# Kernel optimization log

Measured on AMD Instinct MI355X. Metric: run time of the kernel, lower is better.

Reference implementation:

```python
import jax, jax.numpy as jnp
import numpy as np

N, B, T, E = 16384, 8, 32, 262144
D, H = 256, 8
HD = D // H

def _ln(x, g, b, eps=1e-5):
    m = x.mean(-1, keepdims=True)
    va = x.var(-1, keepdims=True)
    return (x - m) * jax.lax.rsqrt(va + eps) * g + b

def setup_inputs():
    key = jax.random.key(0)
    ks = jax.random.split(key, 40)
    rn = lambda i, sh, s=0.02: jax.random.normal(ks[i], sh, jnp.float32) * s
    inp = {}
    inp['x'] = jax.random.normal(ks[0], (N, D), jnp.float32)
    inp['edge_index'] = jax.random.randint(ks[1], (2, E), 0, N)
    inp['edge_attr'] = jax.random.normal(ks[2], (E, D), jnp.float32)
    inp['v'] = jax.random.normal(ks[3], (B, T, D), jnp.float32)
    inp['batch'] = jnp.sort(jax.random.randint(ks[4], (N,), 0, B))
    ones = lambda sh: jnp.ones(sh, jnp.float32)
    zeros = lambda sh: jnp.zeros(sh, jnp.float32)
    # LayerNorms
    inp['n1_g'], inp['n1_b'] = ones((D,)), zeros((D,))
    inp['vn_g'], inp['vn_b'] = ones((D,)), zeros((D,))
    inp['n3_g'], inp['n3_b'] = ones((D,)), zeros((D,))
    inp['n4_g'], inp['n4_b'] = ones((D,)), zeros((D,))
    # GINEConv: eps (train_eps, init 0) + MLP [D, 2D, D] with layer_norm+gelu on hidden
    inp['gine_eps'] = jnp.float32(0.0)
    inp['g_w1'], inp['g_b1'] = rn(5, (2 * D, D)), zeros((2 * D,))
    inp['g_lng'], inp['g_lnb'] = ones((2 * D,)), zeros((2 * D,))
    inp['g_w2'], inp['g_b2'] = rn(6, (D, 2 * D)), zeros((D,))
    # GatedResidual gammas (init 1e-5)
    inp['gamma1'] = jnp.full((D,), 1e-5, jnp.float32)
    inp['gamma2'] = jnp.full((D,), 1e-5, jnp.float32)
    inp['gamma3'] = jnp.full((D,), 1e-5, jnp.float32)
    # MultiheadAttention (packed in_proj)
    inp['mha_in_w'], inp['mha_in_b'] = rn(7, (3 * D, D)), zeros((3 * D,))
    inp['mha_out_w'], inp['mha_out_b'] = rn(8, (D, D)), zeros((D,))
    # node->token cross attention projections
    inp['q_w'], inp['q_b'] = rn(9, (D, D)), zeros((D,))
    inp['kv_w'], inp['kv_b'] = rn(10, (2 * D, D)), zeros((2 * D,))
    inp['o_w'], inp['o_b'] = rn(11, (D, D)), zeros((D,))
    # FFN MLP [D, 4D, D] (eval-mode batch_norm == identity with default stats)
    inp['f_w1'], inp['f_b1'] = rn(12, (4 * D, D)), zeros((4 * D,))
    inp['f_w2'], inp['f_b2'] = rn(13, (D, 4 * D)), zeros((D,))
    return inp

def reference(x, edge_index, edge_attr, v, batch,
              n1_g, n1_b, vn_g, vn_b, n3_g, n3_b, n4_g, n4_b,
              gine_eps, g_w1, g_b1, g_lng, g_lnb, g_w2, g_b2,
              gamma1, gamma2, gamma3,
              mha_in_w, mha_in_b, mha_out_w, mha_out_b,
              q_w, q_b, kv_w, kv_b, o_w, o_b,
              f_w1, f_b1, f_w2, f_b2):
    scale = HD ** -0.5
    gelu = lambda t: jax.nn.gelu(t, approximate=False)
    # --- GINEConv on norm1(x) ---
    xn = _ln(x, n1_g, n1_b)
    src, dst = edge_index[0], edge_index[1]
    msg = jax.nn.relu(xn[src] + edge_attr)                      # [E, D]
    agg = jax.ops.segment_sum(msg, dst, num_segments=N)         # [N, D]
    hin = (1.0 + gine_eps) * xn + agg
    h = gelu(_ln(hin @ g_w1.T + g_b1, g_lng, g_lnb)) @ g_w2.T + g_b2
    x = x + gamma1 * h                                          # res1 (drop_path off in eval)
    # --- token self-attention with node summary context ---
    v_res = v
    vn = _ln(v, vn_g, vn_b)
    cnt = jnp.maximum(jax.ops.segment_sum(jnp.ones((N,), x.dtype), batch, num_segments=B), 1.0)
    node_summary = jax.ops.segment_sum(x, batch, num_segments=B) / cnt[:, None]  # [B, D]
    ctx = jnp.concatenate([vn, node_summary[:, None, :]], axis=1)                # [B, T+1, D]
    wq, wk, wv = jnp.split(mha_in_w, 3, axis=0)
    bq, bk, bv = jnp.split(mha_in_b, 3, axis=0)
    qh = (vn @ wq.T + bq).reshape(B, T, H, HD)
    kh = (ctx @ wk.T + bk).reshape(B, T + 1, H, HD)
    vh = (ctx @ wv.T + bv).reshape(B, T + 1, H, HD)
    a = jax.nn.softmax(jnp.einsum('bqhd,bkhd->bhqk', qh, kh) * scale, axis=-1)
    v_upd = jnp.einsum('bhqk,bkhd->bqhd', a, vh).reshape(B, T, D) @ mha_out_w.T + mha_out_b
    v = v_res + gamma2 * v_upd                                  # res2
    # --- node -> token cross attention (gather-expand KV by batch) ---
    xn3 = _ln(x, n3_g, n3_b)
    q = (xn3 @ q_w.T + q_b).reshape(N, H, HD)
    kv = (v @ kv_w.T + kv_b).reshape(B, T, 2, H, HD)
    k, val = kv[:, :, 0], kv[:, :, 1]                           # [B, T, H, HD]
    k_exp, val_exp = k[batch], val[batch]                       # [N, T, H, HD]
    scores = jnp.einsum('nhd,nthd->nht', q, k_exp) * scale
    attn = jax.nn.softmax(scores, axis=-1)                      # scatter_softmax w/ all-zero idx == softmax over t
    attn_out = jnp.einsum('nht,nthd->nhd', attn, val_exp).reshape(N, D)
    x = x + gamma3 * (attn_out @ o_w.T + o_b)                   # res3
    # --- FFN ---
    xn4 = _ln(x, n4_g, n4_b)
    x = x + (gelu(xn4 @ f_w1.T + f_b1) @ f_w2.T + f_b2)
    return (x, v)
```

## Files before the change

### kernel.cpp

```cpp
#include <hip/hip_runtime.h>
#include <math.h>

#define NN 16384
#define EE 262144
#define BB 8
#define TT 32
#define DD 256
#define HH 8
#define HDD 32

typedef __bf16 bf16;
typedef __bf16 bf16x8 __attribute__((ext_vector_type(8)));
typedef __bf16 bf16x4 __attribute__((ext_vector_type(4)));
typedef float f32x4 __attribute__((ext_vector_type(4)));

#define GM_F32 0
#define GM_BF16 1
#define GM_GELU 2
#define GM_RES 3
#define GM_RES2 4

__device__ __forceinline__ float gelu_f(float v) {
  return 0.5f * v * (1.f + erff(v * 0.70710678118654752440f));
}

struct Cast9 {
  const float* src[9];
  bf16* dst[9];
  int blk_start[10];
};

__global__ __launch_bounds__(256) void cast9(Cast9 c) {
  int blk = blockIdx.x;
  int s = 0;
  while (blk >= c.blk_start[s + 1]) ++s;
  int local = blk - c.blk_start[s];
  int i = local * 1024 + threadIdx.x * 4;
  const float4 f = *(const float4*)(c.src[s] + i);
  bf16x4 o;
  o[0] = (bf16)f.x; o[1] = (bf16)f.y; o[2] = (bf16)f.z; o[3] = (bf16)f.w;
  *(bf16x4*)(c.dst[s] + i) = o;
}

__global__ __launch_bounds__(256) void zero_bufs(int* __restrict__ deg,
                                                 float* __restrict__ summary,
                                                 float* __restrict__ cntf) {
  int b = blockIdx.x;
  if (b < 64) deg[b * 256 + threadIdx.x] = 0;
  else if (b < 72) summary[(b - 64) * 256 + threadIdx.x] = 0.f;
  else if (threadIdx.x < BB) cntf[threadIdx.x] = 0.f;
}

__global__ __launch_bounds__(256) void ln_rows(const float* __restrict__ in,
                                               const float* __restrict__ g,
                                               const float* __restrict__ b,
                                               bf16* __restrict__ out, int C, int do_gelu) {
  int row = blockIdx.x;
  int t = threadIdx.x;
  const float* x = in + (size_t)row * C;
  int nc = C >> 8;
  float lv[2];
  float s = 0.f, s2 = 0.f;
  for (int j = 0; j < nc; ++j) {
    float v = x[j * 256 + t];
    lv[j] = v;
    s += v;
    s2 += v * v;
  }
#pragma unroll
  for (int o = 32; o > 0; o >>= 1) {
    s += __shfl_down(s, o, 64);
    s2 += __shfl_down(s2, o, 64);
  }
  __shared__ float red[8];
  int wv = t >> 6;
  if ((t & 63) == 0) { red[wv] = s; red[4 + wv] = s2; }
  __syncthreads();
  s = red[0] + red[1] + red[2] + red[3];
  s2 = red[4] + red[5] + red[6] + red[7];
  float m = s / C;
  float rs = rsqrtf(s2 / C - m * m + 1e-5f);
  for (int j = 0; j < nc; ++j) {
    int c = j * 256 + t;
    float v = (lv[j] - m) * rs * g[c] + b[c];
    if (do_gelu) v = gelu_f(v);
    out[(size_t)row * C + c] = (bf16)v;
  }
}

__global__ __launch_bounds__(256) void deg_count(const int* __restrict__ ei, int* __restrict__ deg) {
  int e = blockIdx.x * 256 + threadIdx.x;
  if (e < EE) atomicAdd(&deg[ei[EE + e]], 1);
}

__global__ __launch_bounds__(1024) void scan16k(const int* __restrict__ deg,
                                                int* __restrict__ offs, int* __restrict__ woff) {
  __shared__ int part[1024];
  int t = threadIdx.x;
  int base = t * 16;
  int v[16];
  int s = 0;
#pragma unroll
  for (int j = 0; j < 16; ++j) { v[j] = deg[base + j]; s += v[j]; }
  part[t] = s;
  __syncthreads();
  for (int o = 1; o < 1024; o <<= 1) {
    int x = (t >= o) ? part[t - o] : 0;
    __syncthreads();
    part[t] += x;
    __syncthreads();
  }
  int excl = part[t] - s;
#pragma unroll
  for (int j = 0; j < 16; ++j) {
    offs[base + j] = excl;
    woff[base + j] = excl;
    excl += v[j];
  }
  if (t == 1023) offs[NN] = part[1023];
}

__global__ __launch_bounds__(256) void csr_fill(const int* __restrict__ ei, int* __restrict__ woff,
                                                int2* __restrict__ csr2) {
  int e = blockIdx.x * 256 + threadIdx.x;
  if (e < EE) {
    int d = ei[EE + e];
    int s = ei[e];
    int p = atomicAdd(&woff[d], 1);
    csr2[p] = make_int2(e, s);
  }
}

__global__ __launch_bounds__(256) void gine_agg(const float* __restrict__ eattr,
                                                const bf16* __restrict__ xn,
                                                const int* __restrict__ offs,
                                                const int2* __restrict__ csr2,
                                                const float* __restrict__ epsp,
                                                bf16* __restrict__ hin) {
  __shared__ f32x4 red[4][64];
  int n = blockIdx.x;
  int wave = threadIdx.x >> 6, lane = threadIdx.x & 63;
  int s0 = offs[n], s1 = offs[n + 1];
  f32x4 acc = {0.f, 0.f, 0.f, 0.f};
  int i = s0 + wave;
  int2 es = (i < s1) ? csr2[i] : make_int2(0, 0);
  for (; i < s1; i += 4) {
    int2 cur = es;
    int inext = i + 4;
    if (inext < s1) es = csr2[inext];
    float4 ea = *(const float4*)(eattr + (size_t)cur.x * DD + lane * 4);
    bf16x4 xv = *(const bf16x4*)(xn + (size_t)cur.y * DD + lane * 4);
    acc[0] += fmaxf((float)xv[0] + ea.x, 0.f);
    acc[1] += fmaxf((float)xv[1] + ea.y, 0.f);
    acc[2] += fmaxf((float)xv[2] + ea.z, 0.f);
    acc[3] += fmaxf((float)xv[3] + ea.w, 0.f);
  }
  red[wave][lane] = acc;
  __syncthreads();
  if (wave == 0) {
    f32x4 a = red[0][lane];
    f32x4 a1 = red[1][lane], a2 = red[2][lane], a3 = red[3][lane];
    bf16x4 xs = *(const bf16x4*)(xn + (size_t)n * DD + lane * 4);
    float e1 = 1.f + epsp[0];
    bf16x4 o;
#pragma unroll
    for (int j = 0; j < 4; ++j)
      o[j] = (bf16)(e1 * (float)xs[j] + a[j] + a1[j] + a2[j] + a3[j]);
    *(bf16x4*)(hin + (size_t)n * DD + lane * 4) = o;
  }
}

__global__ __launch_bounds__(256) void gemm_bt(const bf16* __restrict__ A,
                                               const bf16* __restrict__ W,
                                               const float* __restrict__ bias,
                                               int M, int K, int NC, int mode,
                                               const float* __restrict__ res,
                                               const float* __restrict__ gamma,
                                               float* __restrict__ outf,
                                               bf16* __restrict__ outb) {
  int wave = threadIdx.x >> 6;
  int lane = threadIdx.x & 63;
  int qd = lane >> 4;
  int l16 = lane & 15;
  int r0 = blockIdx.y * 128 + wave * 32;
  int c0 = blockIdx.x * 64;
  int ar0 = r0 + l16;       if (ar0 >= M) ar0 = M - 1;
  int ar1 = r0 + 16 + l16;  if (ar1 >= M) ar1 = M - 1;
  const bf16* Ap0 = A + (size_t)ar0 * K + qd * 8;
  const bf16* Ap1 = A + (size_t)ar1 * K + qd * 8;
  const bf16* Wp = W + (size_t)(c0 + l16) * K + qd * 8;
  size_t K16 = (size_t)16 * K;
  f32x4 acc00 = {0.f, 0.f, 0.f, 0.f};
  f32x4 acc01 = acc00, acc02 = acc00, acc03 = acc00;
  f32x4 acc10 = acc00, acc11 = acc00, acc12 = acc00, acc13 = acc00;
  for (int k = 0; k < K; k += 32) {
    bf16x8 a0 = *(const bf16x8*)(Ap0 + k);
    bf16x8 a1 = *(const bf16x8*)(Ap1 + k);
    bf16x8 b0 = *(const bf16x8*)(Wp + k);
    bf16x8 b1 = *(const bf16x8*)(Wp + K16 + k);
    bf16x8 b2 = *(const bf16x8*)(Wp + 2 * K16 + k);
    bf16x8 b3 = *(const bf16x8*)(Wp + 3 * K16 + k);
    acc00 = __builtin_amdgcn_mfma_f32_16x16x32_bf16(a0, b0, acc00, 0, 0, 0);
    acc01 = __builtin_amdgcn_mfma_f32_16x16x32_bf16(a0, b1, acc01, 0, 0, 0);
    acc02 = __builtin_amdgcn_mfma_f32_16x16x32_bf16(a0, b2, acc02, 0, 0, 0);
    acc03 = __builtin_amdgcn_mfma_f32_16x16x32_bf16(a0, b3, acc03, 0, 0, 0);
    acc10 = __builtin_amdgcn_mfma_f32_16x16x32_bf16(a1, b0, acc10, 0, 0, 0);
    acc11 = __builtin_amdgcn_mfma_f32_16x16x32_bf16(a1, b1, acc11, 0, 0, 0);
    acc12 = __builtin_amdgcn_mfma_f32_16x16x32_bf16(a1, b2, acc12, 0, 0, 0);
    acc13 = __builtin_amdgcn_mfma_f32_16x16x32_bf16(a1, b3, acc13, 0, 0, 0);
  }
  f32x4 accs[2][4] = {{acc00, acc01, acc02, acc03}, {acc10, acc11, acc12, acc13}};
#pragma unroll
  for (int s = 0; s < 2; ++s) {
#pragma unroll
    for (int c = 0; c < 4; ++c) {
      int col = c0 + c * 16 + l16;
      float bv = bias[col];
#pragma unroll
      for (int i = 0; i < 4; ++i) {
        int row = r0 + s * 16 + qd * 4 + i;
        if (row >= M) continue;
        size_t idx = (size_t)row * NC + col;
        float v = accs[s][c][i] + bv;
        if (mode == GM_F32) outf[idx] = v;
        else if (mode == GM_BF16) outb[idx] = (bf16)v;
        else if (mode == GM_GELU) outb[idx] = (bf16)gelu_f(v);
        else {
          float g = gamma ? gamma[col] : 1.f;
          float r = res[idx] + g * v;
          outf[idx] = r;
          if (mode == GM_RES2) outb[idx] = (bf16)r;
        }
      }
    }
  }
}

__global__ __launch_bounds__(256) void cnt_kernel(const int* __restrict__ batch, float* __restrict__ cntf) {
  __shared__ int hist[BB];
  if (threadIdx.x < BB) hist[threadIdx.x] = 0;
  __syncthreads();
  int n = blockIdx.x * 256 + threadIdx.x;
  if (n < NN) atomicAdd(&hist[batch[n]], 1);
  __syncthreads();
  if (threadIdx.x < BB) {
    int h = hist[threadIdx.x];
    if (h) atomicAdd(&cntf[threadIdx.x], (float)h);
  }
}

__global__ __launch_bounds__(256) void seg_sum(const float* __restrict__ x1,
                                               const int* __restrict__ batch,
                                               float* __restrict__ summary) {
  int r0 = blockIdx.x * 64;
  int t = threadIdx.x;
  float acc = 0.f;
  int curb = batch[r0];
  for (int i = 0; i < 64; ++i) {
    int r = r0 + i;
    int b = batch[r];
    if (b != curb) {
      atomicAdd(&summary[(size_t)curb * DD + t], acc);
      acc = 0.f;
      curb = b;
    }
    acc += x1[(size_t)r * DD + t];
  }
  atomicAdd(&summary[(size_t)curb * DD + t], acc);
}

__global__ __launch_bounds__(256) void build_ctx(const float* __restrict__ summary,
                                                 const float* __restrict__ cntf,
                                                 const bf16* __restrict__ vn,
                                                 bf16* __restrict__ ctx) {
  int r = blockIdx.x, t = threadIdx.x;
  int b = r / (TT + 1), k = r % (TT + 1);
  float val;
  if (k < TT) val = (float)vn[((size_t)(b * TT + k)) * DD + t];
  else val = summary[(size_t)b * DD + t] / fmaxf(cntf[b], 1.f);
  ctx[(size_t)r * DD + t] = (bf16)val;
}

__global__ __launch_bounds__(256) void mha_small(const float* __restrict__ qh,
                                                 const float* __restrict__ kvh,
                                                 bf16* __restrict__ vatt) {
  int b = blockIdx.x;
  int h = threadIdx.x >> 5, qi = threadIdx.x & 31;
  const float scale = 0.17677669529663687f;
  float sc[TT + 1];
  float mx = -1e30f;
  const float* qp = qh + ((size_t)(b * TT + qi)) * DD + h * HDD;
#pragma unroll
  for (int k = 0; k < TT + 1; ++k) {
    const float* kp = kvh + ((size_t)(b * (TT + 1) + k)) * 512 + h * HDD;
    float s = 0.f;
#pragma unroll
    for (int d = 0; d < HDD; ++d) s += qp[d] * kp[d];
    s *= scale;
    sc[k] = s;
    mx = fmaxf(mx, s);
  }
  float sum = 0.f;
#pragma unroll
  for (int k = 0; k < TT + 1; ++k) {
    sc[k] = __expf(sc[k] - mx);
    sum += sc[k];
  }
  float inv = 1.f / sum;
#pragma unroll
  for (int d = 0; d < HDD; ++d) {
    float o = 0.f;
#pragma unroll
    for (int k = 0; k < TT + 1; ++k)
      o += sc[k] * kvh[((size_t)(b * (TT + 1) + k)) * 512 + 256 + h * HDD + d];
    vatt[((size_t)(b * TT + qi)) * DD + h * HDD + d] = (bf16)(o * inv);
  }
}

__global__ __launch_bounds__(256) void cross_attn(const bf16* __restrict__ qx,
                                                  const float* __restrict__ kvx,
                                                  const int* __restrict__ batch,
                                                  bf16* __restrict__ attnout) {
  __shared__ float v_lds[TT * DD];
  int tid = threadIdx.x;
  int n0 = blockIdx.x * 16;
  int b0 = batch[n0];
  for (int i = tid; i < TT * DD; i += 256) {
    int t = i >> 8, c = i & 255;
    v_lds[i] = kvx[((size_t)(b0 * TT + t)) * 512 + 256 + c];
  }
  int h = tid >> 5, lt = tid & 31;
  float kreg[HDD];
  {
    const float* kp = kvx + ((size_t)(b0 * TT + lt)) * 512 + h * HDD;
#pragma unroll
    for (int d = 0; d < HDD; ++d) kreg[d] = kp[d];
  }
  __syncthreads();
  const float scale = 0.17677669529663687f;
  for (int ni = 0; ni < 16; ++ni) {
    int n = n0 + ni;
    int b = batch[n];
    const bf16* qp = qx + (size_t)n * DD + h * HDD;
    float s = 0.f;
    if (b == b0) {
#pragma unroll
      for (int d = 0; d < HDD; ++d) s += (float)qp[d] * kreg[d];
    } else {
      const float* kp = kvx + ((size_t)(b * TT + lt)) * 512 + h * HDD;
#pragma unroll
      for (int d = 0; d < HDD; ++d) s += (float)qp[d] * kp[d];
    }
    s *= scale;
    float mx = s;
#pragma unroll
    for (int o = 16; o > 0; o >>= 1) mx = fmaxf(mx, __shfl_xor(mx, o, 32));
    float e = __expf(s - mx);
    float sum = e;
#pragma unroll
    for (int o = 16; o > 0; o >>= 1) sum += __shfl_xor(sum, o, 32);
    float a = e / sum;
    float o_acc = 0.f;
    int base_lane = (h & 1) << 5;
    if (b == b0) {
#pragma unroll
      for (int t = 0; t < TT; ++t) {
        float at = __shfl(a, base_lane + t, 64);
        o_acc += at * v_lds[t * DD + h * HDD + lt];
      }
    } else {
#pragma unroll
      for (int t = 0; t < TT; ++t) {
        float at = __shfl(a, base_lane + t, 64);
        o_acc += at * kvx[((size_t)(b * TT + t)) * 512 + 256 + h * HDD + lt];
      }
    }
    attnout[(size_t)n * DD + h * HDD + lt] = (bf16)o_acc;
  }
}

extern "C" void kernel_launch(void* const* d_in, const int* in_sizes, int n_in,
                              void* d_out, int out_size, void* d_ws, size_t ws_size,
                              hipStream_t stream) {
  const float* x = (const float*)d_in[0];
  const int* ei = (const int*)d_in[1];
  const float* eattr = (const float*)d_in[2];
  const float* v = (const float*)d_in[3];
  const int* batch = (const int*)d_in[4];
  const float* n1_g = (const float*)d_in[5];
  const float* n1_b = (const float*)d_in[6];
  const float* vn_g = (const float*)d_in[7];
  const float* vn_b = (const float*)d_in[8];
  const float* n3_g = (const float*)d_in[9];
  const float* n3_b = (const float*)d_in[10];
  const float* n4_g = (const float*)d_in[11];
  const float* n4_b = (const float*)d_in[12];
  const float* gine_eps = (const float*)d_in[13];
  const float* g_w1 = (const float*)d_in[14];
  const float* g_b1 = (const float*)d_in[15];
  const float* g_lng = (const float*)d_in[16];
  const float* g_lnb = (const float*)d_in[17];
  const float* g_w2 = (const float*)d_in[18];
  const float* g_b2 = (const float*)d_in[19];
  const float* gamma1 = (const float*)d_in[20];
  const float* gamma2 = (const float*)d_in[21];
  const float* gamma3 = (const float*)d_in[22];
  const float* mha_in_w = (const float*)d_in[23];
  const float* mha_in_b = (const float*)d_in[24];
  const float* mha_out_w = (const float*)d_in[25];
  const float* mha_out_b = (const float*)d_in[26];
  const float* q_w = (const float*)d_in[27];
  const float* q_b = (const float*)d_in[28];
  const float* kv_w = (const float*)d_in[29];
  const float* kv_b = (const float*)d_in[30];
  const float* o_w = (const float*)d_in[31];
  const float* o_b = (const float*)d_in[32];
  const float* f_w1 = (const float*)d_in[33];
  const float* f_b1 = (const float*)d_in[34];
  const float* f_w2 = (const float*)d_in[35];
  const float* f_b2 = (const float*)d_in[36];

  float* out_x = (float*)d_out;
  float* out_v = (float*)d_out + (size_t)NN * DD;

  char* wsp = (char*)d_ws;
  size_t off = 0;
  auto alloc = [&](size_t bytes) -> void* {
    void* p = wsp + off;
    off += (bytes + 255) & ~(size_t)255;
    return p;
  };
  float* t1f = (float*)alloc(33554432);
  bf16* u_bf = (bf16*)t1f;
  bf16* xn_bf = (bf16*)alloc(8388608);
  bf16* qx_bf = xn_bf;
  bf16* t1g_bf = (bf16*)alloc(16777216);
  float* x2f = (float*)t1g_bf;
  float* x1f = (float*)alloc(16777216);
  bf16* hin_bf = (bf16*)alloc(8388608);
  bf16* xn3_bf = hin_bf;
  bf16* att_bf = (bf16*)alloc(8388608);
  bf16* xn4_bf = att_bf;
  int* deg = (int*)alloc(NN * 4);
  int* offs = (int*)alloc((NN + 1) * 4);
  int* woff = (int*)alloc(NN * 4);
  int2* csr2 = (int2*)alloc((size_t)EE * 8);
  float* summary = (float*)alloc(BB * DD * 4);
  float* cntf = (float*)alloc(BB * 4);
  bf16* vn_bf = (bf16*)alloc(BB * TT * DD * 2);
  bf16* ctx_bf = (bf16*)alloc(BB * (TT + 1) * DD * 2);
  float* qhf = (float*)alloc(BB * TT * DD * 4);
  float* kvhf = (float*)alloc(BB * (TT + 1) * 512 * 4);
  bf16* vatt_bf = (bf16*)alloc(BB * TT * DD * 2);
  bf16* vout_bf = (bf16*)alloc(BB * TT * DD * 2);
  float* kvxf = (float*)alloc(BB * TT * 512 * 4);
  bf16* wbuf = (bf16*)alloc((size_t)1310720 * 2);

  bf16* g_w1b = wbuf;
  bf16* g_w2b = g_w1b + 131072;
  bf16* mha_in_wb = g_w2b + 131072;
  bf16* mha_out_wb = mha_in_wb + 196608;
  bf16* q_wb = mha_out_wb + 65536;
  bf16* kv_wb = q_wb + 65536;
  bf16* o_wb = kv_wb + 131072;
  bf16* f_w1b = o_wb + 65536;
  bf16* f_w2b = f_w1b + 262144;

  Cast9 cj;
  cj.src[0] = g_w1; cj.dst[0] = g_w1b;
  cj.src[1] = g_w2; cj.dst[1] = g_w2b;
  cj.src[2] = mha_in_w; cj.dst[2] = mha_in_wb;
  cj.src[3] = mha_out_w; cj.dst[3] = mha_out_wb;
  cj.src[4] = q_w; cj.dst[4] = q_wb;
  cj.src[5] = kv_w; cj.dst[5] = kv_wb;
  cj.src[6] = o_w; cj.dst[6] = o_wb;
  cj.src[7] = f_w1; cj.dst[7] = f_w1b;
  cj.src[8] = f_w2; cj.dst[8] = f_w2b;
  int bs[10] = {0, 128, 256, 448, 512, 576, 704, 768, 1024, 1280};
  for (int i = 0; i < 10; ++i) cj.blk_start[i] = bs[i];
  cast9<<<1280, 256, 0, stream>>>(cj);
  zero_bufs<<<73, 256, 0, stream>>>(deg, summary, cntf);

  ln_rows<<<NN, 256, 0, stream>>>(x, n1_g, n1_b, xn_bf, DD, 0);

  deg_count<<<EE / 256, 256, 0, stream>>>(ei, deg);
  scan16k<<<1, 1024, 0, stream>>>(deg, offs, woff);
  csr_fill<<<EE / 256, 256, 0, stream>>>(ei, woff, csr2);

  gine_agg<<<NN, 256, 0, stream>>>(eattr, xn_bf, offs, csr2, gine_eps, hin_bf);

  gemm_bt<<<dim3(8, 128), 256, 0, stream>>>(hin_bf, g_w1b, g_b1, NN, 256, 512, GM_F32,
                                            nullptr, nullptr, t1f, nullptr);
  ln_rows<<<NN, 256, 0, stream>>>(t1f, g_lng, g_lnb, t1g_bf, 512, 1);
  gemm_bt<<<dim3(4, 128), 256, 0, stream>>>(t1g_bf, g_w2b, g_b2, NN, 512, 256, GM_RES,
                                            x, gamma1, x1f, nullptr);

  cnt_kernel<<<NN / 256, 256, 0, stream>>>(batch, cntf);
  seg_sum<<<NN / 64, 256, 0, stream>>>(x1f, batch, summary);

  ln_rows<<<BB * TT, 256, 0, stream>>>(v, vn_g, vn_b, vn_bf, DD, 0);
  build_ctx<<<BB * (TT + 1), 256, 0, stream>>>(summary, cntf, vn_bf, ctx_bf);
  gemm_bt<<<dim3(4, 2), 256, 0, stream>>>(vn_bf, mha_in_wb, mha_in_b, BB * TT, 256, 256,
                                          GM_F32, nullptr, nullptr, qhf, nullptr);
  gemm_bt<<<dim3(8, 3), 256, 0, stream>>>(ctx_bf, mha_in_wb + (size_t)256 * 256,
                                          mha_in_b + 256, BB * (TT + 1), 256, 512,
                                          GM_F32, nullptr, nullptr, kvhf, nullptr);
  mha_small<<<BB, 256, 0, stream>>>(qhf, kvhf, vatt_bf);
  gemm_bt<<<dim3(4, 2), 256, 0, stream>>>(vatt_bf, mha_out_wb, mha_out_b, BB * TT, 256, 256,
                                          GM_RES2, v, gamma2, out_v, vout_bf);

  gemm_bt<<<dim3(8, 2), 256, 0, stream>>>(vout_bf, kv_wb, kv_b, BB * TT, 256, 512,
                                          GM_F32, nullptr, nullptr, kvxf, nullptr);
  ln_rows<<<NN, 256, 0, stream>>>(x1f, n3_g, n3_b, xn3_bf, DD, 0);
  gemm_bt<<<dim3(4, 128), 256, 0, stream>>>(xn3_bf, q_wb, q_b, NN, 256, 256, GM_BF16,
                                            nullptr, nullptr, nullptr, qx_bf);
  cross_attn<<<NN / 16, 256, 0, stream>>>(qx_bf, kvxf, batch, att_bf);
  gemm_bt<<<dim3(4, 128), 256, 0, stream>>>(att_bf, o_wb, o_b, NN, 256, 256, GM_RES,
                                            x1f, gamma3, x2f, nullptr);

  ln_rows<<<NN, 256, 0, stream>>>(x2f, n4_g, n4_b, xn4_bf, DD, 0);
  gemm_bt<<<dim3(16, 128), 256, 0, stream>>>(xn4_bf, f_w1b, f_b1, NN, 256, 1024, GM_GELU,
                                             nullptr, nullptr, nullptr, u_bf);
  gemm_bt<<<dim3(4, 128), 256, 0, stream>>>(u_bf, f_w2b, f_b2, NN, 1024, 256, GM_RES,
                                            x2f, nullptr, out_x, nullptr);
}
```

Measured before the change: 959.7 us.

## Merge independent small kernels into combined launches and double-buffer GEMM loads

Several independent kernels (weight casts, two LayerNorms, batch histogram, degree count) are folded into one prologue launch dispatched by block index. Seg-sum is merged with the n3 LayerNorm, the ctx build with the q projection GEMM, and the gine W1 GEMM with the small MHA q GEMM, which cuts launch count and per-kernel tail idle time. The GEMM inner loop is also unrolled by two with explicit register double-buffering so global loads for the next K step are issued before the current MFMAs. Zeroing now uses a single memset. The costs are higher register pressure in the GEMM and heterogeneous blocks sharing one launch.

```diff
diff --git a/kernel.cpp b/kernel.cpp
--- a/kernel.cpp
+++ b/kernel.cpp
@@ -24,73 +24,70 @@
   return 0.5f * v * (1.f + erff(v * 0.70710678118654752440f));
 }
 
-struct Cast9 {
-  const float* src[9];
-  bf16* dst[9];
-  int blk_start[10];
-};
-
-__global__ __launch_bounds__(256) void cast9(Cast9 c) {
-  int blk = blockIdx.x;
-  int s = 0;
-  while (blk >= c.blk_start[s + 1]) ++s;
-  int local = blk - c.blk_start[s];
-  int i = local * 1024 + threadIdx.x * 4;
-  const float4 f = *(const float4*)(c.src[s] + i);
-  bf16x4 o;
-  o[0] = (bf16)f.x; o[1] = (bf16)f.y; o[2] = (bf16)f.z; o[3] = (bf16)f.w;
-  *(bf16x4*)(c.dst[s] + i) = o;
-}
-
-__global__ __launch_bounds__(256) void zero_bufs(int* __restrict__ deg,
-                                                 float* __restrict__ summary,
-                                                 float* __restrict__ cntf) {
-  int b = blockIdx.x;
-  if (b < 64) deg[b * 256 + threadIdx.x] = 0;
-  else if (b < 72) summary[(b - 64) * 256 + threadIdx.x] = 0.f;
-  else if (threadIdx.x < BB) cntf[threadIdx.x] = 0.f;
-}
-
-__global__ __launch_bounds__(256) void ln_rows(const float* __restrict__ in,
-                                               const float* __restrict__ g,
-                                               const float* __restrict__ b,
-                                               bf16* __restrict__ out, int C, int do_gelu) {
-  int row = blockIdx.x;
+__device__ __forceinline__ void ln256(const float* __restrict__ xr,
+                                      const float* __restrict__ g,
+                                      const float* __restrict__ bb,
+                                      bf16* __restrict__ o, float* red) {
   int t = threadIdx.x;
-  const float* x = in + (size_t)row * C;
-  int nc = C >> 8;
-  float lv[2];
-  float s = 0.f, s2 = 0.f;
-  for (int j = 0; j < nc; ++j) {
-    float v = x[j * 256 + t];
-    lv[j] = v;
-    s += v;
-    s2 += v * v;
-  }
-#pragma unroll
-  for (int o = 32; o > 0; o >>= 1) {
-    s += __shfl_down(s, o, 64);
-    s2 += __shfl_down(s2, o, 64);
-  }
-  __shared__ float red[8];
+  float v = xr[t];
+  float s = v, s2 = v * v;
+#pragma unroll
+  for (int off = 32; off > 0; off >>= 1) {
+    s += __shfl_down(s, off, 64);
+    s2 += __shfl_down(s2, off, 64);
+  }
   int wv = t >> 6;
   if ((t & 63) == 0) { red[wv] = s; red[4 + wv] = s2; }
   __syncthreads();
   s = red[0] + red[1] + red[2] + red[3];
   s2 = red[4] + red[5] + red[6] + red[7];
-  float m = s / C;
-  float rs = rsqrtf(s2 / C - m * m + 1e-5f);
-  for (int j = 0; j < nc; ++j) {
-    int c = j * 256 + t;
-    float v = (lv[j] - m) * rs * g[c] + b[c];
-    if (do_gelu) v = gelu_f(v);
-    out[(size_t)row * C + c] = (bf16)v;
-  }
-}
-
-__global__ __launch_bounds__(256) void deg_count(const int* __restrict__ ei, int* __restrict__ deg) {
-  int e = blockIdx.x * 256 + threadIdx.x;
-  if (e < EE) atomicAdd(&deg[ei[EE + e]], 1);
+  float m = s * (1.f / 256.f);
+  float rs = rsqrtf(s2 * (1.f / 256.f) - m * m + 1e-5f);
+  o[t] = (bf16)((v - m) * rs * g[t] + bb[t]);
+}
+
+struct Pro {
+  const float* wsrc[9];
+  bf16* wdst[9];
+  int wblk[10];
+  const float* x; const float* n1_g; const float* n1_b; bf16* xn;
+  const float* v; const float* vn_g; const float* vn_b; bf16* vn;
+  const int* batch; float* cntf;
+  const int* ei; int* deg;
+};
+
+__global__ __launch_bounds__(256) void prologue(Pro p) {
+  __shared__ float red[8];
+  __shared__ int hist[BB];
+  int b = blockIdx.x, t = threadIdx.x;
+  if (b < 1280) {
+    int s = 0;
+    while (b >= p.wblk[s + 1]) ++s;
+    int i = (b - p.wblk[s]) * 1024 + t * 4;
+    const float4 f = *(const float4*)(p.wsrc[s] + i);
+    bf16x4 o;
+    o[0] = (bf16)f.x; o[1] = (bf16)f.y; o[2] = (bf16)f.z; o[3] = (bf16)f.w;
+    *(bf16x4*)(p.wdst[s] + i) = o;
+  } else if (b < 17664) {
+    size_t r = b - 1280;
+    ln256(p.x + r * 256, p.n1_g, p.n1_b, p.xn + r * 256, red);
+  } else if (b < 17920) {
+    size_t r = b - 17664;
+    ln256(p.v + r * 256, p.vn_g, p.vn_b, p.vn + r * 256, red);
+  } else if (b < 17984) {
+    if (t < BB) hist[t] = 0;
+    __syncthreads();
+    int n = (b - 17920) * 256 + t;
+    atomicAdd(&hist[p.batch[n]], 1);
+    __syncthreads();
+    if (t < BB) {
+      int h = hist[t];
+      if (h) atomicAdd(&p.cntf[t], (float)h);
+    }
+  } else {
+    int e = (b - 17984) * 256 + t;
+    atomicAdd(&p.deg[p.ei[EE + e]], 1);
+  }
 }
 
 __global__ __launch_bounds__(1024) void scan16k(const int* __restrict__ deg,
@@ -170,115 +167,174 @@
   }
 }
 
-__global__ __launch_bounds__(256) void gemm_bt(const bf16* __restrict__ A,
-                                               const bf16* __restrict__ W,
-                                               const float* __restrict__ bias,
-                                               int M, int K, int NC, int mode,
-                                               const float* __restrict__ res,
-                                               const float* __restrict__ gamma,
-                                               float* __restrict__ outf,
-                                               bf16* __restrict__ outb) {
+struct GemmP {
+  const bf16* A; const bf16* W; const float* bias;
+  int M, K, NC, mode;
+  const float* res; const float* gamma;
+  float* outf; bf16* outb;
+};
+
+__device__ __forceinline__ void gemm_core(const GemmP p, int bx, int by) {
   int wave = threadIdx.x >> 6;
   int lane = threadIdx.x & 63;
   int qd = lane >> 4;
   int l16 = lane & 15;
-  int r0 = blockIdx.y * 128 + wave * 32;
-  int c0 = blockIdx.x * 64;
-  int ar0 = r0 + l16;       if (ar0 >= M) ar0 = M - 1;
-  int ar1 = r0 + 16 + l16;  if (ar1 >= M) ar1 = M - 1;
-  const bf16* Ap0 = A + (size_t)ar0 * K + qd * 8;
-  const bf16* Ap1 = A + (size_t)ar1 * K + qd * 8;
-  const bf16* Wp = W + (size_t)(c0 + l16) * K + qd * 8;
-  size_t K16 = (size_t)16 * K;
+  int r0 = by * 128 + wave * 32;
+  int c0 = bx * 64;
+  int ar0 = r0 + l16;       if (ar0 >= p.M) ar0 = p.M - 1;
+  int ar1 = r0 + 16 + l16;  if (ar1 >= p.M) ar1 = p.M - 1;
+  const bf16* Ap0 = p.A + (size_t)ar0 * p.K + qd * 8;
+  const bf16* Ap1 = p.A + (size_t)ar1 * p.K + qd * 8;
+  const bf16* Wp = p.W + (size_t)(c0 + l16) * p.K + qd * 8;
+  size_t K16 = (size_t)16 * p.K;
   f32x4 acc00 = {0.f, 0.f, 0.f, 0.f};
   f32x4 acc01 = acc00, acc02 = acc00, acc03 = acc00;
   f32x4 acc10 = acc00, acc11 = acc00, acc12 = acc00, acc13 = acc00;
-  for (int k = 0; k < K; k += 32) {
-    bf16x8 a0 = *(const bf16x8*)(Ap0 + k);
-    bf16x8 a1 = *(const bf16x8*)(Ap1 + k);
-    bf16x8 b0 = *(const bf16x8*)(Wp + k);
-    bf16x8 b1 = *(const bf16x8*)(Wp + K16 + k);
-    bf16x8 b2 = *(const bf16x8*)(Wp + 2 * K16 + k);
-    bf16x8 b3 = *(const bf16x8*)(Wp + 3 * K16 + k);
-    acc00 = __builtin_amdgcn_mfma_f32_16x16x32_bf16(a0, b0, acc00, 0, 0, 0);
-    acc01 = __builtin_amdgcn_mfma_f32_16x16x32_bf16(a0, b1, acc01, 0, 0, 0);
-    acc02 = __builtin_amdgcn_mfma_f32_16x16x32_bf16(a0, b2, acc02, 0, 0, 0);
-    acc03 = __builtin_amdgcn_mfma_f32_16x16x32_bf16(a0, b3, acc03, 0, 0, 0);
-    acc10 = __builtin_amdgcn_mfma_f32_16x16x32_bf16(a1, b0, acc10, 0, 0, 0);
-    acc11 = __builtin_amdgcn_mfma_f32_16x16x32_bf16(a1, b1, acc11, 0, 0, 0);
-    acc12 = __builtin_amdgcn_mfma_f32_16x16x32_bf16(a1, b2, acc12, 0, 0, 0);
-    acc13 = __builtin_amdgcn_mfma_f32_16x16x32_bf16(a1, b3, acc13, 0, 0, 0);
-  }
+  bf16x8 a0, a1, b0, b1, b2, b3, na0, na1, nb0, nb1, nb2, nb3;
+
+#define GLOADS(A0, A1, B0, B1, B2, B3, kk)                \
+  A0 = *(const bf16x8*)(Ap0 + (kk));                      \
+  A1 = *(const bf16x8*)(Ap1 + (kk));                      \
+  B0 = *(const bf16x8*)(Wp + (kk));                       \
+  B1 = *(const bf16x8*)(Wp + K16 + (kk));                 \
+  B2 = *(const bf16x8*)(Wp + 2 * K16 + (kk));             \
+  B3 = *(const bf16x8*)(Wp + 3 * K16 + (kk));
+#define GMFMAS(A0, A1, B0, B1, B2, B3)                                  \
+  acc00 = __builtin_amdgcn_mfma_f32_16x16x32_bf16(A0, B0, acc00, 0, 0, 0); \
+  acc01 = __builtin_amdgcn_mfma_f32_16x16x32_bf16(A0, B1, acc01, 0, 0, 0); \
+  acc02 = __builtin_amdgcn_mfma_f32_16x16x32_bf16(A0, B2, acc02, 0, 0, 0); \
+  acc03 = __builtin_amdgcn_mfma_f32_16x16x32_bf16(A0, B3, acc03, 0, 0, 0); \
+  acc10 = __builtin_amdgcn_mfma_f32_16x16x32_bf16(A1, B0, acc10, 0, 0, 0); \
+  acc11 = __builtin_amdgcn_mfma_f32_16x16x32_bf16(A1, B1, acc11, 0, 0, 0); \
+  acc12 = __builtin_amdgcn_mfma_f32_16x16x32_bf16(A1, B2, acc12, 0, 0, 0); \
+  acc13 = __builtin_amdgcn_mfma_f32_16x16x32_bf16(A1, B3, acc13, 0, 0, 0);
+
+  GLOADS(a0, a1, b0, b1, b2, b3, 0)
+  int k = 32;
+  for (; k + 32 < p.K; k += 64) {
+    GLOADS(na0, na1, nb0, nb1, nb2, nb3, k)
+    GMFMAS(a0, a1, b0, b1, b2, b3)
+    GLOADS(a0, a1, b0, b1, b2, b3, k + 32)
+    GMFMAS(na0, na1, nb0, nb1, nb2, nb3)
+  }
+  GLOADS(na0, na1, nb0, nb1, nb2, nb3, k)
+  GMFMAS(a0, a1, b0, b1, b2, b3)
+  GMFMAS(na0, na1, nb0, nb1, nb2, nb3)
+#undef GLOADS
+#undef GMFMAS
+
   f32x4 accs[2][4] = {{acc00, acc01, acc02, acc03}, {acc10, acc11, acc12, acc13}};
 #pragma unroll
   for (int s = 0; s < 2; ++s) {
 #pragma unroll
     for (int c = 0; c < 4; ++c) {
       int col = c0 + c * 16 + l16;
-      float bv = bias[col];
+      float bv = p.bias[col];
 #pragma unroll
       for (int i = 0; i < 4; ++i) {
         int row = r0 + s * 16 + qd * 4 + i;
-        if (row >= M) continue;
-        size_t idx = (size_t)row * NC + col;
+        if (row >= p.M) continue;
+        size_t idx = (size_t)row * p.NC + col;
         float v = accs[s][c][i] + bv;
-        if (mode == GM_F32) outf[idx] = v;
-        else if (mode == GM_BF16) outb[idx] = (bf16)v;
-        else if (mode == GM_GELU) outb[idx] = (bf16)gelu_f(v);
+        if (p.mode == GM_F32) p.outf[idx] = v;
+        else if (p.mode == GM_BF16) p.outb[idx] = (bf16)v;
+        else if (p.mode == GM_GELU) p.outb[idx] = (bf16)gelu_f(v);
         else {
-          float g = gamma ? gamma[col] : 1.f;
-          float r = res[idx] + g * v;
-          outf[idx] = r;
-          if (mode == GM_RES2) outb[idx] = (bf16)r;
+          float g = p.gamma ? p.gamma[col] : 1.f;
+          float r = p.res[idx] + g * v;
+          p.outf[idx] = r;
+          if (p.mode == GM_RES2) p.outb[idx] = (bf16)r;
         }
       }
     }
   }
 }
 
-__global__ __launch_bounds__(256) void cnt_kernel(const int* __restrict__ batch, float* __restrict__ cntf) {
-  __shared__ int hist[BB];
-  if (threadIdx.x < BB) hist[threadIdx.x] = 0;
+__global__ __launch_bounds__(256) void gemm_one(GemmP p, int nbx) {
+  gemm_core(p, blockIdx.x % nbx, blockIdx.x / nbx);
+}
+
+__global__ __launch_bounds__(256) void gemm_dual(GemmP p0, int nblk0, int nbx0,
+                                                 GemmP p1, int nbx1) {
+  int b = blockIdx.x;
+  if (b < nblk0) gemm_core(p0, b % nbx0, b / nbx0);
+  else {
+    b -= nblk0;
+    gemm_core(p1, b % nbx1, b / nbx1);
+  }
+}
+
+__global__ __launch_bounds__(256) void ln512_gelu(const float* __restrict__ in,
+                                                  const float* __restrict__ g,
+                                                  const float* __restrict__ b,
+                                                  bf16* __restrict__ out) {
+  int row = blockIdx.x;
+  int t = threadIdx.x;
+  const float* x = in + (size_t)row * 512;
+  float v0 = x[t], v1 = x[256 + t];
+  float s = v0 + v1, s2 = v0 * v0 + v1 * v1;
+#pragma unroll
+  for (int o = 32; o > 0; o >>= 1) {
+    s += __shfl_down(s, o, 64);
+    s2 += __shfl_down(s2, o, 64);
+  }
+  __shared__ float red[8];
+  int wv = t >> 6;
+  if ((t & 63) == 0) { red[wv] = s; red[4 + wv] = s2; }
   __syncthreads();
-  int n = blockIdx.x * 256 + threadIdx.x;
-  if (n < NN) atomicAdd(&hist[batch[n]], 1);
-  __syncthreads();
-  if (threadIdx.x < BB) {
-    int h = hist[threadIdx.x];
-    if (h) atomicAdd(&cntf[threadIdx.x], (float)h);
-  }
-}
-
-__global__ __launch_bounds__(256) void seg_sum(const float* __restrict__ x1,
-                                               const int* __restrict__ batch,
-                                               float* __restrict__ summary) {
-  int r0 = blockIdx.x * 64;
-  int t = threadIdx.x;
-  float acc = 0.f;
-  int curb = batch[r0];
-  for (int i = 0; i < 64; ++i) {
-    int r = r0 + i;
-    int b = batch[r];
-    if (b != curb) {
-      atomicAdd(&summary[(size_t)curb * DD + t], acc);
-      acc = 0.f;
-      curb = b;
+  s = red[0] + red[1] + red[2] + red[3];
+  s2 = red[4] + red[5] + red[6] + red[7];
+  float m = s * (1.f / 512.f);
+  float rs = rsqrtf(s2 * (1.f / 512.f) - m * m + 1e-5f);
+  out[(size_t)row * 512 + t] = (bf16)gelu_f((v0 - m) * rs * g[t] + b[t]);
+  out[(size_t)row * 512 + 256 + t] = (bf16)gelu_f((v1 - m) * rs * g[256 + t] + b[256 + t]);
+}
+
+__global__ __launch_bounds__(256) void mid1(const float* __restrict__ x1,
+                                            const int* __restrict__ batch,
+                                            float* __restrict__ summary,
+                                            const float* __restrict__ n3_g,
+                                            const float* __restrict__ n3_b,
+                                            bf16* __restrict__ xn3) {
+  __shared__ float red[8];
+  int b = blockIdx.x, t = threadIdx.x;
+  if (b < 256) {
+    int r0 = b * 64;
+    float acc = 0.f;
+    int curb = batch[r0];
+    for (int i = 0; i < 64; ++i) {
+      int r = r0 + i;
+      int bb = batch[r];
+      if (bb != curb) {
+        atomicAdd(&summary[(size_t)curb * DD + t], acc);
+        acc = 0.f;
+        curb = bb;
+      }
+      acc += x1[(size_t)r * DD + t];
     }
-    acc += x1[(size_t)r * DD + t];
-  }
-  atomicAdd(&summary[(size_t)curb * DD + t], acc);
-}
-
-__global__ __launch_bounds__(256) void build_ctx(const float* __restrict__ summary,
-                                                 const float* __restrict__ cntf,
-                                                 const bf16* __restrict__ vn,
-                                                 bf16* __restrict__ ctx) {
-  int r = blockIdx.x, t = threadIdx.x;
-  int b = r / (TT + 1), k = r % (TT + 1);
-  float val;
-  if (k < TT) val = (float)vn[((size_t)(b * TT + k)) * DD + t];
-  else val = summary[(size_t)b * DD + t] / fmaxf(cntf[b], 1.f);
-  ctx[(size_t)r * DD + t] = (bf16)val;
+    atomicAdd(&summary[(size_t)curb * DD + t], acc);
+  } else {
+    size_t r = b - 256;
+    ln256(x1 + r * 256, n3_g, n3_b, xn3 + r * 256, red);
+  }
+}
+
+__global__ __launch_bounds__(256) void mid2(const float* __restrict__ summary,
+                                            const float* __restrict__ cntf,
+                                            const bf16* __restrict__ vn,
+                                            bf16* __restrict__ ctx,
+                                            GemmP qp) {
+  int b = blockIdx.x, t = threadIdx.x;
+  if (b < BB * (TT + 1)) {
+    int bb = b / (TT + 1), k = b % (TT + 1);
+    float val;
+    if (k < TT) val = (float)vn[((size_t)(bb * TT + k)) * DD + t];
+    else val = summary[(size_t)bb * DD + t] / fmaxf(cntf[bb], 1.f);
+    ctx[(size_t)b * DD + t] = (bf16)val;
+  } else {
+    int l = b - BB * (TT + 1);
+    gemm_core(qp, l % 4, l / 4);
+  }
 }
 
 __global__ __launch_bounds__(256) void mha_small(const float* __restrict__ qh,
@@ -377,6 +433,15 @@
     }
     attnout[(size_t)n * DD + h * HDD + lt] = (bf16)o_acc;
   }
+}
+
+__global__ __launch_bounds__(256) void ln4_k(const float* __restrict__ in,
+                                             const float* __restrict__ g,
+                                             const float* __restrict__ b,
+                                             bf16* __restrict__ out) {
+  __shared__ float red[8];
+  size_t r = blockIdx.x;
+  ln256(in + r * 256, g, b, out + r * 256, red);
 }
 
 extern "C" void kernel_launch(void* const* d_in, const int* in_sizes, int n_in,
@@ -442,11 +507,11 @@
   bf16* att_bf = (bf16*)alloc(8388608);
   bf16* xn4_bf = att_bf;
   int* deg = (int*)alloc(NN * 4);
+  float* summary = (float*)alloc(BB * DD * 4);
+  float* cntf = (float*)alloc(BB * 4);
   int* offs = (int*)alloc((NN + 1) * 4);
   int* woff = (int*)alloc(NN * 4);
   int2* csr2 = (int2*)alloc((size_t)EE * 8);
-  float* summary = (float*)alloc(BB * DD * 4);
-  float* cntf = (float*)alloc(BB * 4);
   bf16* vn_bf = (bf16*)alloc(BB * TT * DD * 2);
   bf16* ctx_bf = (bf16*)alloc(BB * (TT + 1) * DD * 2);
   float* qhf = (float*)alloc(BB * TT * DD * 4);
@@ -466,61 +531,67 @@
   bf16* f_w1b = o_wb + 65536;
   bf16* f_w2b = f_w1b + 262144;
 
-  Cast9 cj;
-  cj.src[0] = g_w1; cj.dst[0] = g_w1b;
-  cj.src[1] = g_w2; cj.dst[1] = g_w2b;
-  cj.src[2] = mha_in_w; cj.dst[2] = mha_in_wb;
-  cj.src[3] = mha_out_w; cj.dst[3] = mha_out_wb;
-  cj.src[4] = q_w; cj.dst[4] = q_wb;
-  cj.src[5] = kv_w; cj.dst[5] = kv_wb;
-  cj.src[6] = o_w; cj.dst[6] = o_wb;
-  cj.src[7] = f_w1; cj.dst[7] = f_w1b;
-  cj.src[8] = f_w2; cj.dst[8] = f_w2b;
+  hipMemsetAsync(deg, 0, NN * 4 + BB * DD * 4 + 256, stream);
+
+  Pro pr;
+  pr.wsrc[0] = g_w1; pr.wdst[0] = g_w1b;
+  pr.wsrc[1] = g_w2; pr.wdst[1] = g_w2b;
+  pr.wsrc[2] = mha_in_w; pr.wdst[2] = mha_in_wb;
+  pr.wsrc[3] = mha_out_w; pr.wdst[3] = mha_out_wb;
+  pr.wsrc[4] = q_w; pr.wdst[4] = q_wb;
+  pr.wsrc[5] = kv_w; pr.wdst[5] = kv_wb;
+  pr.wsrc[6] = o_w; pr.wdst[6] = o_wb;
+  pr.wsrc[7] = f_w1; pr.wdst[7] = f_w1b;
+  pr.wsrc[8] = f_w2; pr.wdst[8] = f_w2b;
   int bs[10] = {0, 128, 256, 448, 512, 576, 704, 768, 1024, 1280};
-  for (int i = 0; i < 10; ++i) cj.blk_start[i] = bs[i];
-  cast9<<<1280, 256, 0, stream>>>(cj);
-  zero_bufs<<<73, 256, 0, stream>>>(deg, summary, cntf);
-
-  ln_rows<<<NN, 256, 0, stream>>>(x, n1_g, n1_b, xn_bf, DD, 0);
-
-  deg_count<<<EE / 256, 256, 0, stream>>>(ei, deg);
+  for (int i = 0; i < 10; ++i) pr.wblk[i] = bs[i];
+  pr.x = x; pr.n1_g = n1_g; pr.n1_b = n1_b; pr.xn = xn_bf;
+  pr.v = v; pr.vn_g = vn_g; pr.vn_b = vn_b; pr.vn = vn_bf;
+  pr.batch = batch; pr.cntf = cntf;
+  pr.ei = ei; pr.deg = deg;
+  prologue<<<19008, 256, 0, stream>>>(pr);
+
   scan16k<<<1, 1024, 0, stream>>>(deg, offs, woff);
   csr_fill<<<EE / 256, 256, 0, stream>>>(ei, woff, csr2);
 
   gine_agg<<<NN, 256, 0, stream>>>(eattr, xn_bf, offs, csr2, gine_eps, hin_bf);
 
-  gemm_bt<<<dim3(8, 128), 256, 0, stream>>>(hin_bf, g_w1b, g_b1, NN, 256, 512, GM_F32,
-                                            nullptr, nullptr, t1f, nullptr);
-  ln_rows<<<NN, 256, 0, stream>>>(t1f, g_lng, g_lnb, t1g_bf, 512, 1);
-  gemm_bt<<<dim3(4, 128), 256, 0, stream>>>(t1g_bf, g_w2b, g_b2, NN, 512, 256, GM_RES,
-                                            x, gamma1, x1f, nullptr);
-
-  cnt_kernel<<<NN / 256, 256, 0, stream>>>(batch, cntf);
-  seg_sum<<<NN / 64, 256, 0, stream>>>(x1f, batch, summary);
-
-  ln_rows<<<BB * TT, 256, 0, stream>>>(v, vn_g, vn_b, vn_bf, DD, 0);
-  build_ctx<<<BB * (TT + 1), 256, 0, stream>>>(summary, cntf, vn_bf, ctx_bf);
-  gemm_bt<<<dim3(4, 2), 256, 0, stream>>>(vn_bf, mha_in_wb, mha_in_b, BB * TT, 256, 256,
-                                          GM_F32, nullptr, nullptr, qhf, nullptr);
-  gemm_bt<<<dim3(8, 3), 256, 0, stream>>>(ctx_bf, mha_in_wb + (size_t)256 * 256,
-                                          mha_in_b + 256, BB * (TT + 1), 256, 512,
-                                          GM_F32, nullptr, nullptr, kvhf, nullptr);
+  GemmP j_gw1 = {hin_bf, g_w1b, g_b1, NN, 256, 512, GM_F32, nullptr, nullptr, t1f, nullptr};
+  GemmP j_qh = {vn_bf, mha_in_wb, mha_in_b, BB * TT, 256, 256, GM_F32, nullptr, nullptr, qhf, nullptr};
+  gemm_dual<<<1024 + 8, 256, 0, stream>>>(j_gw1, 1024, 8, j_qh, 4);
+
+  ln512_gelu<<<NN, 256, 0, stream>>>(t1f, g_lng, g_lnb, t1g_bf);
+
+  GemmP j_gw2 = {t1g_bf, g_w2b, g_b2, NN, 512, 256, GM_RES, x, gamma1, x1f, nullptr};
+  gemm_one<<<512, 256, 0, stream>>>(j_gw2, 4);
+
+  mid1<<<256 + NN, 256, 0, stream>>>(x1f, batch, summary, n3_g, n3_b, xn3_bf);
+
+  GemmP j_q = {xn3_bf, q_wb, q_b, NN, 256, 256, GM_BF16, nullptr, nullptr, nullptr, qx_bf};
+  mid2<<<BB * (TT + 1) + 512, 256, 0, stream>>>(summary, cntf, vn_bf, ctx_bf, j_q);
+
+  GemmP j_kvh = {ctx_bf, mha_in_wb + (size_t)256 * 256, mha_in_b + 256, BB * (TT + 1), 256, 512,
+                 GM_F32, nullptr, nullptr, kvhf, nullptr};
+  gemm_one<<<24, 256, 0, stream>>>(j_kvh, 8);
+
   mha_small<<<BB, 256, 0, stream>>>(qhf, kvhf, vatt_bf);
-  gemm_bt<<<dim3(4, 2), 256, 0, stream>>>(vatt_bf, mha_out_wb, mha_out_b, BB * TT, 256, 256,
-                                          GM_RES2, v, gamma2, out_v, vout_bf);
-
-  gemm_bt<<<dim3(8, 2), 256, 0, stream>>>(vout_bf, kv_wb, kv_b, BB * TT, 256, 512,
-                                          GM_F32, nullptr, nullptr, kvxf, nullptr);
-  ln_rows<<<NN, 256, 0, stream>>>(x1f, n3_g, n3_b, xn3_bf, DD, 0);
-  gemm_bt<<<dim3(4, 128), 256, 0, stream>>>(xn3_bf, q_wb, q_b, NN, 256, 256, GM_BF16,
-                                            nullptr, nullptr, nullptr, qx_bf);
+
+  GemmP j_mo = {vatt_bf, mha_out_wb, mha_out_b, BB * TT, 256, 256, GM_RES2, v, gamma2, out_v, vout_bf};
+  gemm_one<<<8, 256, 0, stream>>>(j_mo, 4);
+
+  GemmP j_kv = {vout_bf, kv_wb, kv_b, BB * TT, 256, 512, GM_F32, nullptr, nullptr, kvxf, nullptr};
+  gemm_one<<<16, 256, 0, stream>>>(j_kv, 8);
+
   cross_attn<<<NN / 16, 256, 0, stream>>>(qx_bf, kvxf, batch, att_bf);
-  gemm_bt<<<dim3(4, 128), 256, 0, stream>>>(att_bf, o_wb, o_b, NN, 256, 256, GM_RES,
-                                            x1f, gamma3, x2f, nullptr);
-
-  ln_rows<<<NN, 256, 0, stream>>>(x2f, n4_g, n4_b, xn4_bf, DD, 0);
-  gemm_bt<<<dim3(16, 128), 256, 0, stream>>>(xn4_bf, f_w1b, f_b1, NN, 256, 1024, GM_GELU,
-                                             nullptr, nullptr, nullptr, u_bf);
-  gemm_bt<<<dim3(4, 128), 256, 0, stream>>>(u_bf, f_w2b, f_b2, NN, 1024, 256, GM_RES,
-                                            x2f, nullptr, out_x, nullptr);
-}
+
+  GemmP j_o = {att_bf, o_wb, o_b, NN, 256, 256, GM_RES, x1f, gamma3, x2f, nullptr};
+  gemm_one<<<512, 256, 0, stream>>>(j_o, 4);
+
+  ln4_k<<<NN, 256, 0, stream>>>(x2f, n4_g, n4_b, xn4_bf);
+
+  GemmP j_f1 = {xn4_bf, f_w1b, f_b1, NN, 256, 1024, GM_GELU, nullptr, nullptr, nullptr, u_bf};
+  gemm_one<<<2048, 256, 0, stream>>>(j_f1, 16);
+
+  GemmP j_f2 = {u_bf, f_w2b, f_b2, NN, 1024, 256, GM_RES, x2f, nullptr, out_x, nullptr};
+  gemm_one<<<512, 256, 0, stream>>>(j_f2, 4);
+}
```

New measurement: 944.0 us. About the same (-1.6%).
